# Performance work log

Measured on AMD Instinct MI355X. Metric: run time of the kernel, lower is better.

## Reference

```python
import jax, jax.numpy as jnp
import numpy as np

B, S, D = 4, 2048, 2048
H, NOPE, ROPE, V, KVR = 16, 128, 64, 128, 512
QK = NOPE + ROPE  # 192
THETA = 10000.0
EPS = 1e-6


def setup_inputs() -> dict:
    key = jax.random.key(0)
    ks = jax.random.split(key, 6)
    x = jax.random.normal(ks[0], (B, S, D), jnp.float32)
    wq = jax.random.normal(ks[1], (H * QK, D), jnp.float32) * 0.02
    wkv_a = jax.random.normal(ks[2], (KVR + ROPE, D), jnp.float32) * 0.02
    kv_norm_w = jnp.ones((KVR,), jnp.float32)
    wkv_b = jax.random.normal(ks[3], (H * (NOPE + V), KVR), jnp.float32) * 0.02
    wo = jax.random.normal(ks[4], (D, H * V), jnp.float32) * 0.02
    # rotary frequency tables (interleaved-pair convention, pairs = ROPE//2)
    pos = np.arange(S, dtype=np.float64)
    inv = 1.0 / (THETA ** (np.arange(0, ROPE, 2, dtype=np.float64) / ROPE))
    ang = pos[:, None] * inv[None, :]  # [S, ROPE//2]
    freqs_cos = jnp.asarray(np.cos(ang), jnp.float32)
    freqs_sin = jnp.asarray(np.sin(ang), jnp.float32)
    return dict(x=x, wq=wq, wkv_a=wkv_a, kv_norm_w=kv_norm_w,
                wkv_b=wkv_b, wo=wo, freqs_cos=freqs_cos, freqs_sin=freqs_sin)


def _rope(x, cos, sin):
    # x: [B, S, H, d] with interleaved complex pairs along last dim
    x1, x2 = x[..., 0::2], x[..., 1::2]
    c = cos[None, :, None, :]
    s = sin[None, :, None, :]
    y1 = x1 * c - x2 * s
    y2 = x1 * s + x2 * c
    return jnp.stack([y1, y2], axis=-1).reshape(x.shape)


def _rmsnorm(x, w):
    var = jnp.mean(jnp.square(x), axis=-1, keepdims=True)
    return x * jax.lax.rsqrt(var + EPS) * w


def reference(x, wq, wkv_a, kv_norm_w, wkv_b, wo, freqs_cos, freqs_sin):
    softmax_scale = QK ** (-0.5)  # mscale path inactive (S <= original_seq_len)
    # query projection (q_lora_rank == 0 -> direct)
    q = (x @ wq.T).reshape(B, S, H, QK)
    q_nope, q_pe = q[..., :NOPE], q[..., NOPE:]
    q_pe = _rope(q_pe, freqs_cos, freqs_sin)
    # latent KV projection + decoupled rope key
    kv = x @ wkv_a.T  # [B, S, KVR + ROPE]
    kv_c = _rmsnorm(kv[..., :KVR], kv_norm_w)  # latent KV cache entries
    k_pe = _rope(kv[..., None, KVR:], freqs_cos, freqs_sin)[:, :, 0]  # [B,S,ROPE]
    # absorb wkv_b's nope block into q (attention runs in 512-dim latent space)
    wkv_b_r = wkv_b.reshape(H, NOPE + V, KVR)
    q_lat = jnp.einsum('bshd,hdc->bshc', q_nope, wkv_b_r[:, :NOPE])
    scores = (jnp.einsum('bshc,btc->bsht', q_lat, kv_c)
              + jnp.einsum('bshr,btr->bsht', q_pe, k_pe)) * softmax_scale
    mask = jnp.triu(jnp.full((S, S), -1e9, jnp.float32), k=1)  # causal
    attn = jax.nn.softmax(scores + mask[None, :, None, :], axis=-1)
    out = jnp.einsum('bsht,btc->bshc', attn, kv_c)  # latent output
    out = jnp.einsum('bshc,hdc->bshd', out, wkv_b_r[:, NOPE:])  # un-absorb V
    return out.reshape(B, S, H * V) @ wo.T
```

## Files before the change

### kernel.cpp

```cpp
#include <hip/hip_runtime.h>
#include <hip/hip_bf16.h>
#include <cstdint>

typedef __bf16 bf16;
typedef __bf16 bf16x8 __attribute__((ext_vector_type(8)));
typedef float f32x4 __attribute__((ext_vector_type(4)));
typedef unsigned int u32x4 __attribute__((ext_vector_type(4)));

#define B_ 4
#define S_ 2048
#define D_ 2048
#define H_ 16
#define NOPE_ 128
#define ROPE_ 64
#define V_ 128
#define KVR_ 512
#define QK_ 192
#define KD_ 576

__device__ __forceinline__ bf16 tobf(float f) {
  unsigned u = __float_as_uint(f);
  u += 0x7fffu + ((u >> 16) & 1u);
  unsigned short s = (unsigned short)(u >> 16);
  return *reinterpret_cast<bf16*>(&s);
}
__device__ __forceinline__ float tof(bf16 v) {
  unsigned short s = *reinterpret_cast<unsigned short*>(&v);
  return __uint_as_float(((unsigned)s) << 16);
}

__global__ void cast_bf16(const float* __restrict__ in, bf16* __restrict__ out, long n) {
  long i = ((long)blockIdx.x * 256 + threadIdx.x) * 8;
  if (i >= n) return;
  float4 a = *(const float4*)(in + i);
  float4 b = *(const float4*)(in + i + 4);
  bf16x8 v;
  v[0] = tobf(a.x); v[1] = tobf(a.y); v[2] = tobf(a.z); v[3] = tobf(a.w);
  v[4] = tobf(b.x); v[5] = tobf(b.y); v[6] = tobf(b.z); v[7] = tobf(b.w);
  *(bf16x8*)(out + i) = v;
}

__global__ void prep_wkvb(const float* __restrict__ w, bf16* __restrict__ wnT, bf16* __restrict__ wv) {
  int tid = blockIdx.x * 256 + threadIdx.x;
  {
    int c = tid & 511, rest = tid >> 9, d = rest & 127, h = rest >> 7;
    wv[tid] = tobf(w[((long)(h * 256 + 128 + d) << 9) + c]);
  }
  {
    int d = tid & 127, rest = tid >> 7, c = rest & 511, h = rest >> 9;
    wnT[tid] = tobf(w[((long)(h * 256 + d) << 9) + c]);
  }
}

template <typename OutT>
__global__ __launch_bounds__(256)
void gemm_bt(const bf16* __restrict__ A, long lda, long aOffZ,
             const bf16* __restrict__ Bm, long ldb, long bOffZ,
             OutT* __restrict__ C, long ldc, long cOffZ,
             int M, int N, int K)
{
  A += aOffZ * blockIdx.z;
  Bm += bOffZ * blockIdx.z;
  C += cOffZ * blockIdx.z;
  const int m0 = blockIdx.y * 128, n0 = blockIdx.x * 128;
  const int tid = threadIdx.x;
  const int wave = tid >> 6, lane = tid & 63, quad = lane >> 4, r = lane & 15;
  const int wm = (wave >> 1) * 64, wn = (wave & 1) * 64;
  __shared__ __align__(16) bf16 As[128][40];
  __shared__ __align__(16) bf16 Bs[128][40];
  f32x4 acc[4][4] = {};
  for (int k0 = 0; k0 < K; k0 += 32) {
    __syncthreads();
#pragma unroll
    for (int it = 0; it < 2; ++it) {
      int idx = tid + it * 256;
      int row = idx >> 2, ch = (idx & 3) * 8;
      long ar = m0 + row; if (ar > (long)M - 1) ar = M - 1;
      *(u32x4*)&As[row][ch] = *(const u32x4*)(A + ar * lda + k0 + ch);
      long br = n0 + row; if (br > (long)N - 1) br = N - 1;
      *(u32x4*)&Bs[row][ch] = *(const u32x4*)(Bm + br * ldb + k0 + ch);
    }
    __syncthreads();
    bf16x8 af[4], bfr[4];
#pragma unroll
    for (int i = 0; i < 4; ++i) af[i] = *(const bf16x8*)&As[wm + i * 16 + r][quad * 8];
#pragma unroll
    for (int j = 0; j < 4; ++j) bfr[j] = *(const bf16x8*)&Bs[wn + j * 16 + r][quad * 8];
#pragma unroll
    for (int i = 0; i < 4; ++i)
#pragma unroll
      for (int j = 0; j < 4; ++j)
        acc[i][j] = __builtin_amdgcn_mfma_f32_16x16x32_bf16(af[i], bfr[j], acc[i][j], 0, 0, 0);
  }
#pragma unroll
  for (int i = 0; i < 4; ++i) {
    int mrow = m0 + wm + i * 16 + quad * 4;
#pragma unroll
    for (int j = 0; j < 4; ++j) {
      int ncol = n0 + wn + j * 16 + r;
      if (ncol < N) {
#pragma unroll
        for (int t = 0; t < 4; ++t) {
          if (mrow + t < M) {
            if constexpr (__is_same(OutT, float))
              C[(long)(mrow + t) * ldc + ncol] = acc[i][j][t];
            else
              C[(long)(mrow + t) * ldc + ncol] = tobf(acc[i][j][t]);
          }
        }
      }
    }
  }
}

__global__ void kv_norm(const float* __restrict__ kvf, const float* __restrict__ w,
                        const float* __restrict__ fcos, const float* __restrict__ fsin,
                        bf16* __restrict__ keff) {
  int row = blockIdx.x * 4 + (threadIdx.x >> 6);
  int lane = threadIdx.x & 63;
  int t = row;
  const float* src = kvf + (long)row * KD_;
  float v[8]; float ss = 0.f;
#pragma unroll
  for (int i = 0; i < 8; ++i) { v[i] = src[lane * 8 + i]; ss += v[i] * v[i]; }
#pragma unroll
  for (int off = 1; off < 64; off <<= 1) ss += __shfl_xor(ss, off, 64);
  float rms = rsqrtf(ss * (1.f / 512.f) + 1e-6f);
  bf16* dst = keff + (long)row * KD_;
#pragma unroll
  for (int i = 0; i < 8; ++i) dst[lane * 8 + i] = tobf(v[i] * rms * w[lane * 8 + i]);
  if (lane < 32) {
    float x1 = src[KVR_ + 2 * lane], x2 = src[KVR_ + 2 * lane + 1];
    float c = fcos[t * 32 + lane], s = fsin[t * 32 + lane];
    dst[KVR_ + 2 * lane]     = tobf(x1 * c - x2 * s);
    dst[KVR_ + 2 * lane + 1] = tobf(x1 * s + x2 * c);
  }
}

__global__ void transpose_kvc(const bf16* __restrict__ keff, bf16* __restrict__ kvcT) {
  int c0 = blockIdx.y * 32, t0 = blockIdx.x * 32;
  __shared__ bf16 tile[32][33];
  int x = threadIdx.x & 31, y = threadIdx.x >> 5;
#pragma unroll
  for (int k = 0; k < 4; ++k) {
    int t = t0 + y + k * 8;
    tile[y + k * 8][x] = keff[(long)t * KD_ + c0 + x];
  }
  __syncthreads();
#pragma unroll
  for (int k = 0; k < 4; ++k) {
    int c = c0 + y + k * 8;
    kvcT[(long)c * S_ + t0 + x] = tile[x][y + k * 8];
  }
}

__global__ void rope_q(const bf16* __restrict__ qb, const float* __restrict__ fcos,
                       const float* __restrict__ fsin, bf16* __restrict__ qeff) {
  long tid = (long)blockIdx.x * 256 + threadIdx.x;
  int i = tid & 31; int h = (tid >> 5) & 15; long bs = tid >> 9; int t = (int)bs;
  const bf16* src = qb + bs * (H_ * QK_) + h * QK_ + NOPE_ + 2 * i;
  float x1 = tof(src[0]), x2 = tof(src[1]);
  float c = fcos[t * 32 + i], s = fsin[t * 32 + i];
  long o = (bs * H_ + h) * KD_ + KVR_ + 2 * i;
  qeff[o]     = tobf(x1 * c - x2 * s);
  qeff[o + 1] = tobf(x1 * s + x2 * c);
}

__global__ __launch_bounds__(256, 2)
void flash_mla(const bf16* __restrict__ Qeff, const bf16* __restrict__ Keff,
               const bf16* __restrict__ kvcT, bf16* __restrict__ Oc)
{
  const int qt = 31 - (blockIdx.x >> 4);
  const int h = blockIdx.x & 15;
  const int s0 = qt * 64;
  const int tid = threadIdx.x;
  const int wave = tid >> 6, lane = tid & 63, quad = lane >> 4, r = lane & 15;
  const int rh = wave & 1, ch = wave >> 1;
  const int nt = 2 * qt + 2;

  __shared__ __align__(16) bf16 Ks[32][584];
  __shared__ __align__(16) bf16 Vs[512][36];
  __shared__ __align__(16) bf16 Pl[64][36];
  __shared__ __align__(16) float alphaL[64];
  __shared__ __align__(16) float linvL[64];
  const float scale = 0.07216878364870323f;

  const int qrow = s0 + 16 * wave + r;
  bf16x8 aq[18];
  const bf16* qptr = Qeff + ((long)qrow * H_ + h) * KD_;
#pragma unroll
  for (int kc = 0; kc < 18; ++kc) aq[kc] = *(const bf16x8*)(qptr + kc * 32 + quad * 8);

  f32x4 o0[16] = {};
  f32x4 o1[16] = {};
  float m_run = -INFINITY, l_run = 0.f;

  for (int kt = 0; kt < nt; ++kt) {
    const int t0 = kt * 32;
    __syncthreads();
#pragma unroll
    for (int i = 0; i < 9; ++i) {
      int c = tid + i * 256;
      int row = c / 72, col = c - row * 72;
      *(u32x4*)&Ks[row][col * 8] = *(const u32x4*)(Keff + (long)(t0 + row) * KD_ + col * 8);
    }
#pragma unroll
    for (int i = 0; i < 8; ++i) {
      int c = tid + i * 256;
      int row = c >> 2, col = c & 3;
      *(u32x4*)&Vs[row][col * 8] = *(const u32x4*)(kvcT + (long)row * S_ + t0 + col * 8);
    }
    __syncthreads();
    f32x4 sacc0 = {}, sacc1 = {};
#pragma unroll
    for (int kc = 0; kc < 18; ++kc) {
      bf16x8 k0 = *(const bf16x8*)&Ks[r][kc * 32 + quad * 8];
      bf16x8 k1 = *(const bf16x8*)&Ks[16 + r][kc * 32 + quad * 8];
      sacc0 = __builtin_amdgcn_mfma_f32_16x16x32_bf16(k0, aq[kc], sacc0, 0, 0, 0);
      sacc1 = __builtin_amdgcn_mfma_f32_16x16x32_bf16(k1, aq[kc], sacc1, 0, 0, 0);
    }
    float s8[8];
#pragma unroll
    for (int tt = 0; tt < 4; ++tt) {
      int ka = t0 + quad * 4 + tt;
      s8[tt]     = (ka      <= qrow) ? sacc0[tt] * scale : -INFINITY;
      s8[4 + tt] = (ka + 16 <= qrow) ? sacc1[tt] * scale : -INFINITY;
    }
    float mx = s8[0];
#pragma unroll
    for (int i = 1; i < 8; ++i) mx = fmaxf(mx, s8[i]);
    mx = fmaxf(mx, __shfl_xor(mx, 16, 64));
    mx = fmaxf(mx, __shfl_xor(mx, 32, 64));
    float mnew = fmaxf(m_run, mx);
    float alpha = __expf(m_run - mnew);
    float ps = 0.f;
#pragma unroll
    for (int i = 0; i < 8; ++i) { float pv = __expf(s8[i] - mnew); s8[i] = pv; ps += pv; }
    ps += __shfl_xor(ps, 16, 64);
    ps += __shfl_xor(ps, 32, 64);
    l_run = l_run * alpha + ps;
    m_run = mnew;
#pragma unroll
    for (int tt = 0; tt < 4; ++tt) {
      Pl[16 * wave + r][quad * 4 + tt]      = tobf(s8[tt]);
      Pl[16 * wave + r][16 + quad * 4 + tt] = tobf(s8[4 + tt]);
    }
    if (quad == 0) alphaL[16 * wave + r] = alpha;
    __syncthreads();
    f32x4 a0 = *(const f32x4*)&alphaL[32 * rh + quad * 4];
    f32x4 a1 = *(const f32x4*)&alphaL[32 * rh + 16 + quad * 4];
#pragma unroll
    for (int j = 0; j < 16; ++j) {
#pragma unroll
      for (int tt = 0; tt < 4; ++tt) { o0[j][tt] *= a0[tt]; o1[j][tt] *= a1[tt]; }
    }
    bf16x8 p0 = *(const bf16x8*)&Pl[32 * rh + r][quad * 8];
    bf16x8 p1 = *(const bf16x8*)&Pl[32 * rh + 16 + r][quad * 8];
#pragma unroll
    for (int j = 0; j < 16; ++j) {
      bf16x8 bv = *(const bf16x8*)&Vs[256 * ch + 16 * j + r][quad * 8];
      o0[j] = __builtin_amdgcn_mfma_f32_16x16x32_bf16(p0, bv, o0[j], 0, 0, 0);
      o1[j] = __builtin_amdgcn_mfma_f32_16x16x32_bf16(p1, bv, o1[j], 0, 0, 0);
    }
  }
  if (quad == 0) linvL[16 * wave + r] = 1.0f / l_run;
  __syncthreads();
  f32x4 li0 = *(const f32x4*)&linvL[32 * rh + quad * 4];
  f32x4 li1 = *(const f32x4*)&linvL[32 * rh + 16 + quad * 4];
#pragma unroll
  for (int tt = 0; tt < 4; ++tt) {
    long row0 = (long)(s0 + 32 * rh + quad * 4 + tt);
    long row1 = row0 + 16;
    bf16* orow0 = Oc + (row0 * H_ + h) * KVR_ + 256 * ch;
    bf16* orow1 = Oc + (row1 * H_ + h) * KVR_ + 256 * ch;
#pragma unroll
    for (int j = 0; j < 16; ++j) {
      orow0[j * 16 + r] = tobf(o0[j][tt] * li0[tt]);
      orow1[j * 16 + r] = tobf(o1[j][tt] * li1[tt]);
    }
  }
}

extern "C" void kernel_launch(void* const* d_in, const int* in_sizes, int n_in,
                              void* d_out, int out_size, void* d_ws, size_t ws_size,
                              hipStream_t stream) {
  (void)in_sizes; (void)n_in; (void)out_size; (void)ws_size;
  const float* x     = (const float*)d_in[0];
  const float* wq    = (const float*)d_in[1];
  const float* wkv_a = (const float*)d_in[2];
  const float* kvw   = (const float*)d_in[3];
  const float* wkv_b = (const float*)d_in[4];
  const float* wo    = (const float*)d_in[5];
  const float* fcos  = (const float*)d_in[6];
  const float* fsin  = (const float*)d_in[7];
  float* out = (float*)d_out;

  char* p = (char*)d_ws;
  auto alloc = [&](size_t bytes) { char* q = p; p += (bytes + 255) & ~(size_t)255; return q; };
  const long MR = (long)B_ * S_;
  bf16* xb   = (bf16*)alloc(MR * D_ * 2);
  bf16* out2 = (bf16*)alloc(MR * D_ * 2);
  bf16* wqb  = (bf16*)alloc((long)H_ * QK_ * D_ * 2);
  bf16* wab  = (bf16*)alloc((long)KD_ * D_ * 2);
  bf16* wob  = (bf16*)alloc((long)D_ * D_ * 2);
  bf16* wbnT = (bf16*)alloc((long)H_ * KVR_ * NOPE_ * 2);
  bf16* wbv  = (bf16*)alloc((long)H_ * V_ * KVR_ * 2);
  float* kvf = (float*)alloc((long)S_ * KD_ * 4);
  bf16* keff = (bf16*)alloc((long)S_ * KD_ * 2);
  bf16* kvcT = (bf16*)alloc((long)KVR_ * S_ * 2);
  bf16* qb   = (bf16*)alloc((long)S_ * H_ * QK_ * 2);
  bf16* qeff = (bf16*)alloc((long)S_ * H_ * KD_ * 2);
  bf16* oc   = (bf16*)alloc((long)S_ * H_ * KVR_ * 2);

  cast_bf16<<<(MR * D_) >> 11, 256, 0, stream>>>(x, xb, MR * D_);
  cast_bf16<<<((long)H_ * QK_ * D_) >> 11, 256, 0, stream>>>(wq, wqb, (long)H_ * QK_ * D_);
  cast_bf16<<<((long)KD_ * D_) >> 11, 256, 0, stream>>>(wkv_a, wab, (long)KD_ * D_);
  cast_bf16<<<((long)D_ * D_) >> 11, 256, 0, stream>>>(wo, wob, (long)D_ * D_);
  prep_wkvb<<<4096, 256, 0, stream>>>(wkv_b, wbnT, wbv);

  for (int b = 0; b < B_; ++b) {
    const bf16* xb_b = xb + (long)b * S_ * D_;
    bf16* out2_b = out2 + (long)b * S_ * D_;
    gemm_bt<float><<<dim3(5, 16, 1), 256, 0, stream>>>(xb_b, D_, 0, wab, D_, 0,
                                                       kvf, KD_, 0, S_, KD_, D_);
    kv_norm<<<S_ / 4, 256, 0, stream>>>(kvf, kvw, fcos, fsin, keff);
    transpose_kvc<<<dim3(S_ / 32, KVR_ / 32, 1), 256, 0, stream>>>(keff, kvcT);
    gemm_bt<bf16><<<dim3(24, 16, 1), 256, 0, stream>>>(xb_b, D_, 0, wqb, D_, 0,
                                                       qb, H_ * QK_, 0, S_, H_ * QK_, D_);
    rope_q<<<(S_ * H_ * 32) / 256, 256, 0, stream>>>(qb, fcos, fsin, qeff);
    gemm_bt<bf16><<<dim3(4, 16, H_), 256, 0, stream>>>(qb, H_ * QK_, QK_,
                                                       wbnT, NOPE_, (long)KVR_ * NOPE_,
                                                       qeff, H_ * KD_, KD_, S_, KVR_, NOPE_);
    flash_mla<<<dim3(512), 256, 0, stream>>>(qeff, keff, kvcT, oc);
    gemm_bt<bf16><<<dim3(1, 16, H_), 256, 0, stream>>>(oc, H_ * KVR_, KVR_,
                                                       wbv, KVR_, (long)V_ * KVR_,
                                                       out2_b, D_, V_, S_, V_, KVR_);
  }
  gemm_bt<float><<<dim3(16, 64, 1), 256, 0, stream>>>(out2, D_, 0, wob, D_, 0,
                                                      out, D_, 0, MR, D_, D_);
}
```

Before: 2.595 ms.

## Double-buffer K tiles with async LDS loads and enlarge flash MLA query tile

The flash MLA kernel now processes 128 query rows per block with 8 waves instead of 64 rows with 4 waves, halving the grid. K tiles are double-buffered in LDS and fetched with global_load_lds async copies using an XOR swizzle. V tiles are prefetched into registers one step ahead, which removes one barrier per iteration and overlaps global loads with the MFMA work. The aim is to hide memory latency and reuse each K/V tile across more query rows, at the cost of higher LDS use (about 125 KB) and coarser causal work imbalance across blocks.

```diff
diff --git a/kernel.cpp b/kernel.cpp
--- a/kernel.cpp
+++ b/kernel.cpp
@@ -4,6 +4,7 @@
 
 typedef __bf16 bf16;
 typedef __bf16 bf16x8 __attribute__((ext_vector_type(8)));
+typedef __bf16 bf16x4 __attribute__((ext_vector_type(4)));
 typedef float f32x4 __attribute__((ext_vector_type(4)));
 typedef unsigned int u32x4 __attribute__((ext_vector_type(4)));
 
@@ -17,6 +18,13 @@
 #define KVR_ 512
 #define QK_ 192
 #define KD_ 576
+
+#define LDS_AS __attribute__((address_space(3)))
+#define GLB_AS __attribute__((address_space(1)))
+
+__device__ __forceinline__ void async16(const bf16* g, bf16* l) {
+  __builtin_amdgcn_global_load_lds((const GLB_AS uint32_t*)g, (LDS_AS uint32_t*)l, 16, 0, 0);
+}
 
 __device__ __forceinline__ bf16 tobf(float f) {
   unsigned u = __float_as_uint(f);
@@ -166,56 +174,77 @@
   qeff[o + 1] = tobf(x1 * s + x2 * c);
 }
 
-__global__ __launch_bounds__(256, 2)
+__global__ __launch_bounds__(512, 2)
 void flash_mla(const bf16* __restrict__ Qeff, const bf16* __restrict__ Keff,
                const bf16* __restrict__ kvcT, bf16* __restrict__ Oc)
 {
-  const int qt = 31 - (blockIdx.x >> 4);
-  const int h = blockIdx.x & 15;
-  const int s0 = qt * 64;
+  const int qt = 15 - (blockIdx.x >> 4);
+  const int h  = blockIdx.x & 15;
+  const int s0 = qt * 128;
   const int tid = threadIdx.x;
   const int wave = tid >> 6, lane = tid & 63, quad = lane >> 4, r = lane & 15;
-  const int rh = wave & 1, ch = wave >> 1;
-  const int nt = 2 * qt + 2;
-
-  __shared__ __align__(16) bf16 Ks[32][584];
-  __shared__ __align__(16) bf16 Vs[512][36];
-  __shared__ __align__(16) bf16 Pl[64][36];
-  __shared__ __align__(16) float alphaL[64];
-  __shared__ __align__(16) float linvL[64];
+  const int rw = wave & 3, cw = wave >> 2;
+  const int nt = 4 * qt + 4;
+
+  __shared__ __align__(16) bf16 Ks[2][32 * 576];
+  __shared__ __align__(16) bf16 Vs[512 * 40];
+  __shared__ __align__(16) bf16 Pl[128 * 40];
+  __shared__ float alphaL[128];
+  __shared__ float linvL[128];
+
+  int koffE[5];
+#pragma unroll
+  for (int i = 0; i < 5; ++i) {
+    int n = (i < 4) ? (i * 512 + tid) : (2048 + (tid & 255));
+    int row = n / 72, p = n - row * 72;
+    int src = p ^ ((row ^ (row >> 3)) & 7);
+    koffE[i] = row * KD_ + src * 8;
+  }
+  int voffG[4], voffL[4];
+#pragma unroll
+  for (int i = 0; i < 4; ++i) {
+    int n = i * 512 + tid;
+    int row = n >> 2, col = (n & 3) * 8;
+    voffG[i] = row * S_ + col;
+    voffL[i] = row * 40 + col;
+  }
+
+  bf16x8 aq[18];
+  {
+    const bf16* qptr = Qeff + ((long)(s0 + 16 * wave + r) * H_ + h) * KD_;
+#pragma unroll
+    for (int kc = 0; kc < 18; ++kc) aq[kc] = *(const bf16x8*)(qptr + kc * 32 + quad * 8);
+  }
+
+  const int sA = (r ^ (r >> 3)) & 7;
+  const int rB = 16 + r;
+  const int sB = (rB ^ (rB >> 3)) & 7;
+  const int qrow = s0 + 16 * wave + r;
   const float scale = 0.07216878364870323f;
 
-  const int qrow = s0 + 16 * wave + r;
-  bf16x8 aq[18];
-  const bf16* qptr = Qeff + ((long)qrow * H_ + h) * KD_;
-#pragma unroll
-  for (int kc = 0; kc < 18; ++kc) aq[kc] = *(const bf16x8*)(qptr + kc * 32 + quad * 8);
-
-  f32x4 o0[16] = {};
-  f32x4 o1[16] = {};
+  f32x4 o0[16] = {}, o1[16] = {};
   float m_run = -INFINITY, l_run = 0.f;
+
+#pragma unroll
+  for (int i = 0; i < 4; ++i)
+    async16(Keff + koffE[i], (bf16*)&Ks[0][(i * 512 + wave * 64) * 8]);
+  if (wave < 4)
+    async16(Keff + koffE[4], (bf16*)&Ks[0][(2048 + wave * 64) * 8]);
+  u32x4 vreg[4];
+#pragma unroll
+  for (int i = 0; i < 4; ++i) vreg[i] = *(const u32x4*)(kvcT + voffG[i]);
 
   for (int kt = 0; kt < nt; ++kt) {
     const int t0 = kt * 32;
+    const int cur = kt & 1;
     __syncthreads();
 #pragma unroll
-    for (int i = 0; i < 9; ++i) {
-      int c = tid + i * 256;
-      int row = c / 72, col = c - row * 72;
-      *(u32x4*)&Ks[row][col * 8] = *(const u32x4*)(Keff + (long)(t0 + row) * KD_ + col * 8);
-    }
-#pragma unroll
-    for (int i = 0; i < 8; ++i) {
-      int c = tid + i * 256;
-      int row = c >> 2, col = c & 3;
-      *(u32x4*)&Vs[row][col * 8] = *(const u32x4*)(kvcT + (long)row * S_ + t0 + col * 8);
-    }
-    __syncthreads();
+    for (int i = 0; i < 4; ++i) *(u32x4*)&Vs[voffL[i]] = vreg[i];
     f32x4 sacc0 = {}, sacc1 = {};
 #pragma unroll
     for (int kc = 0; kc < 18; ++kc) {
-      bf16x8 k0 = *(const bf16x8*)&Ks[r][kc * 32 + quad * 8];
-      bf16x8 k1 = *(const bf16x8*)&Ks[16 + r][kc * 32 + quad * 8];
+      bf16x8 k0 = *(const bf16x8*)&Ks[cur][(r  * 72 + ((4 * kc + quad) ^ sA)) * 8];
+      bf16x8 k1 = *(const bf16x8*)&Ks[cur][(rB * 72 + ((4 * kc + quad) ^ sB)) * 8];
       sacc0 = __builtin_amdgcn_mfma_f32_16x16x32_bf16(k0, aq[kc], sacc0, 0, 0, 0);
       sacc1 = __builtin_amdgcn_mfma_f32_16x16x32_bf16(k1, aq[kc], sacc1, 0, 0, 0);
     }
@@ -240,39 +269,52 @@
     ps += __shfl_xor(ps, 32, 64);
     l_run = l_run * alpha + ps;
     m_run = mnew;
-#pragma unroll
-    for (int tt = 0; tt < 4; ++tt) {
-      Pl[16 * wave + r][quad * 4 + tt]      = tobf(s8[tt]);
-      Pl[16 * wave + r][16 + quad * 4 + tt] = tobf(s8[4 + tt]);
+    {
+      bf16x4 plo, phi;
+#pragma unroll
+      for (int tt = 0; tt < 4; ++tt) { plo[tt] = tobf(s8[tt]); phi[tt] = tobf(s8[4 + tt]); }
+      *(bf16x4*)&Pl[(16 * wave + r) * 40 + quad * 4]      = plo;
+      *(bf16x4*)&Pl[(16 * wave + r) * 40 + 16 + quad * 4] = phi;
     }
     if (quad == 0) alphaL[16 * wave + r] = alpha;
     __syncthreads();
-    f32x4 a0 = *(const f32x4*)&alphaL[32 * rh + quad * 4];
-    f32x4 a1 = *(const f32x4*)&alphaL[32 * rh + 16 + quad * 4];
+    if (kt + 1 < nt) {
+      const bf16* kb = Keff + (long)(t0 + 32) * KD_;
+#pragma unroll
+      for (int i = 0; i < 4; ++i)
+        async16(kb + koffE[i], (bf16*)&Ks[1 - cur][(i * 512 + wave * 64) * 8]);
+      if (wave < 4)
+        async16(kb + koffE[4], (bf16*)&Ks[1 - cur][(2048 + wave * 64) * 8]);
+      const bf16* vb = kvcT + t0 + 32;
+#pragma unroll
+      for (int i = 0; i < 4; ++i) vreg[i] = *(const u32x4*)(vb + voffG[i]);
+    }
+    f32x4 a0 = *(const f32x4*)&alphaL[32 * rw + quad * 4];
+    f32x4 a1 = *(const f32x4*)&alphaL[32 * rw + 16 + quad * 4];
 #pragma unroll
     for (int j = 0; j < 16; ++j) {
 #pragma unroll
       for (int tt = 0; tt < 4; ++tt) { o0[j][tt] *= a0[tt]; o1[j][tt] *= a1[tt]; }
     }
-    bf16x8 p0 = *(const bf16x8*)&Pl[32 * rh + r][quad * 8];
-    bf16x8 p1 = *(const bf16x8*)&Pl[32 * rh + 16 + r][quad * 8];
+    bf16x8 p0 = *(const bf16x8*)&Pl[(32 * rw + r) * 40 + quad * 8];
+    bf16x8 p1 = *(const bf16x8*)&Pl[(32 * rw + 16 + r) * 40 + quad * 8];
 #pragma unroll
     for (int j = 0; j < 16; ++j) {
-      bf16x8 bv = *(const bf16x8*)&Vs[256 * ch + 16 * j + r][quad * 8];
+      bf16x8 bv = *(const bf16x8*)&Vs[(256 * cw + 16 * j + r) * 40 + quad * 8];
       o0[j] = __builtin_amdgcn_mfma_f32_16x16x32_bf16(p0, bv, o0[j], 0, 0, 0);
       o1[j] = __builtin_amdgcn_mfma_f32_16x16x32_bf16(p1, bv, o1[j], 0, 0, 0);
     }
   }
   if (quad == 0) linvL[16 * wave + r] = 1.0f / l_run;
   __syncthreads();
-  f32x4 li0 = *(const f32x4*)&linvL[32 * rh + quad * 4];
-  f32x4 li1 = *(const f32x4*)&linvL[32 * rh + 16 + quad * 4];
+  f32x4 li0 = *(const f32x4*)&linvL[32 * rw + quad * 4];
+  f32x4 li1 = *(const f32x4*)&linvL[32 * rw + 16 + quad * 4];
 #pragma unroll
   for (int tt = 0; tt < 4; ++tt) {
-    long row0 = (long)(s0 + 32 * rh + quad * 4 + tt);
+    long row0 = (long)(s0 + 32 * rw + quad * 4 + tt);
     long row1 = row0 + 16;
-    bf16* orow0 = Oc + (row0 * H_ + h) * KVR_ + 256 * ch;
-    bf16* orow1 = Oc + (row1 * H_ + h) * KVR_ + 256 * ch;
+    bf16* orow0 = Oc + (row0 * H_ + h) * KVR_ + 256 * cw;
+    bf16* orow1 = Oc + (row1 * H_ + h) * KVR_ + 256 * cw;
 #pragma unroll
     for (int j = 0; j < 16; ++j) {
       orow0[j * 16 + r] = tobf(o0[j][tt] * li0[tt]);
@@ -331,7 +373,7 @@
     gemm_bt<bf16><<<dim3(4, 16, H_), 256, 0, stream>>>(qb, H_ * QK_, QK_,
                                                        wbnT, NOPE_, (long)KVR_ * NOPE_,
                                                        qeff, H_ * KD_, KD_, S_, KVR_, NOPE_);
-    flash_mla<<<dim3(512), 256, 0, stream>>>(qeff, keff, kvcT, oc);
+    flash_mla<<<dim3(256), 512, 0, stream>>>(qeff, keff, kvcT, oc);
     gemm_bt<bf16><<<dim3(1, 16, H_), 256, 0, stream>>>(oc, H_ * KVR_, KVR_,
                                                        wbv, KVR_, (long)V_ * KVR_,
                                                        out2_b, D_, V_, S_, V_, KVR_);
```

Result: no change. 2.564 ms (-1.2%).
